# Kernel optimization log

Measured on AMD Instinct MI355X. Metric: run time of the kernel, lower is better.

Reference implementation:

```python
import jax, jax.numpy as jnp
import numpy as np

N = 100000   # nodes
F = 64       # features
K = 5        # filter taps
E = 1600000  # edges per sparse power (avg degree 16)


def setup_inputs() -> dict:
    key = jax.random.key(0)
    k1, k2, k3, k4, k5 = jax.random.split(key, 5)
    x = jax.random.normal(k1, (N, F), dtype=jnp.float32)
    h = jax.random.normal(k2, (K,), dtype=jnp.float32)
    vals = jax.random.normal(k3, (K, E), dtype=jnp.float32)
    rows = jax.random.randint(k4, (K, E), 0, N, dtype=jnp.int32)
    cols = jax.random.randint(k5, (K, E), 0, N, dtype=jnp.int32)
    return {"x": x, "h": h, "vals": vals, "rows": rows, "cols": cols}


def reference(x, h, vals, rows, cols):
    # H = sum_k h[k] * S_k  (COO);  out = H @ x
    # Fuse the weighted sum of K sparse matrices directly into one SpMM:
    # scale each power's values by h[k], flatten all K edge lists, and
    # scatter-add the gathered rows of x.
    n = x.shape[0]
    w = (h[:, None] * vals).reshape(-1)          # [K*E]
    r = rows.reshape(-1)                         # [K*E]
    c = cols.reshape(-1)                         # [K*E]
    contrib = x[c] * w[:, None]                  # [K*E, F] gather + scale
    out = jax.ops.segment_sum(contrib, r, num_segments=n)  # [N, F]
    return out
```

## Files before the change

### kernel.cpp

```cpp
#include <hip/hip_runtime.h>
#include <hip/hip_bf16.h>


#define RPB   64
#define SUB   2
#define GWG   128

static __global__ __launch_bounds__(1024) void count_kernel(
    const int* __restrict__ rows, int* __restrict__ cnt,
    int KE, int NSTREAM, int chunk)
{
    extern __shared__ int hist[];
    const int g = blockIdx.x;
    for (int j = threadIdx.x; j < NSTREAM; j += blockDim.x) hist[j] = 0;
    __syncthreads();
    const int lo = g * chunk;
    const int hi = min(lo + chunk, KE);
    for (int e = lo + threadIdx.x; e < hi; e += blockDim.x) {
        const int r = rows[e];
        atomicAdd(&hist[((r >> 6) << 1) | (r & 1)], 1);
    }
    __syncthreads();
    for (int j = threadIdx.x; j < NSTREAM; j += blockDim.x)
        cnt[(size_t)j * GWG + g] = hist[j];
}

static __global__ __launch_bounds__(GWG) void scan1_kernel(
    int* __restrict__ cnt, int* __restrict__ ssBeg)
{
    __shared__ int tmp[GWG];
    const int s = blockIdx.x;
    const int t = threadIdx.x;
    const int v = cnt[(size_t)s * GWG + t];
    tmp[t] = v;
    __syncthreads();
    for (int d = 1; d < GWG; d <<= 1) {
        int u = (t >= d) ? tmp[t - d] : 0;
        __syncthreads();
        tmp[t] += u;
        __syncthreads();
    }
    cnt[(size_t)s * GWG + t] = tmp[t] - v;
    if (t == GWG - 1) ssBeg[s] = tmp[t];
}

static __global__ __launch_bounds__(1024) void scan2_kernel(
    int* __restrict__ a, int n)
{
    __shared__ int sums[1024];
    const int t = threadIdx.x;
    const int chunk = (n + 1023) >> 10;
    const int lo = t * chunk;
    const int hi = min(lo + chunk, n);
    int s = 0;
    for (int i = lo; i < hi; ++i) s += a[i];
    sums[t] = s;
    __syncthreads();
    for (int d = 1; d < 1024; d <<= 1) {
        int v = (t >= d) ? sums[t - d] : 0;
        __syncthreads();
        sums[t] += v;
        __syncthreads();
    }
    int run = (t > 0) ? sums[t - 1] : 0;
    for (int i = lo; i < hi; ++i) {
        const int cv = a[i];
        a[i] = run;
        run += cv;
    }
    if (t == 1023) a[n] = sums[1023];
}

static __global__ __launch_bounds__(1024) void scan3_kernel(
    int* __restrict__ cnt, const int* __restrict__ ssBeg, int total)
{
    const int i = blockIdx.x * blockDim.x + threadIdx.x;
    if (i < total) cnt[i] += ssBeg[i >> 7];
}

static __global__ __launch_bounds__(1024) void scatter_kernel(
    const int*   __restrict__ rows,
    const int*   __restrict__ cols,
    const float* __restrict__ vals,
    const float* __restrict__ h,
    const int*   __restrict__ cnt,
    int2*        __restrict__ payload,
    int KE, int E, int K, int NSTREAM, int chunk)
{
    extern __shared__ int lcur[];
    const int g = blockIdx.x;
    for (int j = threadIdx.x; j < NSTREAM; j += blockDim.x)
        lcur[j] = cnt[(size_t)j * GWG + g];
    __syncthreads();
    const int lo = g * chunk;
    const int hi = min(lo + chunk, KE);
    if (lo >= hi) return;
    const int k0 = lo / E;
    const int k1 = min((hi - 1) / E, K - 1);
    for (int k = k0; k <= k1; ++k) {
        const float hk = h[k];
        const int s0 = max(lo, k * E);
        const int s1 = min(hi, (k + 1) * E);
        for (int e = s0 + threadIdx.x; e < s1; e += blockDim.x) {
            const int r = rows[e];
            const int st = ((r >> 6) << 1) | (r & 1);
            const int pos = atomicAdd(&lcur[st], 1);
            payload[pos] = make_int2(((r & 63) << 17) | cols[e],
                                     __float_as_int(hk * vals[e]));
        }
    }
}

static __global__ __launch_bounds__(256) void convert_kernel(
    const float* __restrict__ x, ushort* __restrict__ xh, int n4)
{
    const int i = blockIdx.x * blockDim.x + threadIdx.x;
    if (i >= n4) return;
    const float4 v = ((const float4*)x)[i];
    ushort4 o;
    o.x = __bfloat16_as_ushort(__float2bfloat16(v.x));
    o.y = __bfloat16_as_ushort(__float2bfloat16(v.y));
    o.z = __bfloat16_as_ushort(__float2bfloat16(v.z));
    o.w = __bfloat16_as_ushort(__float2bfloat16(v.w));
    ((ushort4*)xh)[i] = o;
}

static __global__ __launch_bounds__(128) void spmv_bf16_kernel(
    const int*    __restrict__ ssBeg,
    const int2*   __restrict__ payload,
    const ushort* __restrict__ xh,
    float*        __restrict__ out,
    int N)
{
    __shared__ float acc[RPB * 64];
    const int b = blockIdx.x;
    for (int i = threadIdx.x; i < RPB * 64; i += 128) acc[i] = 0.f;
    __syncthreads();

    const int lane = threadIdx.x & 63;
    const int wv   = threadIdx.x >> 6;
    const int s    = b * SUB + wv;
    int e        = ssBeg[s];
    const int be = ssBeg[s + 1];

    while (e + 16 <= be) {
        int2 pa[8], pb[8];
        float xa[8], xb[8];
        #pragma unroll
        for (int j = 0; j < 8; ++j) pa[j] = payload[e + j];
        #pragma unroll
        for (int j = 0; j < 8; ++j) pb[j] = payload[e + 8 + j];
        #pragma unroll
        for (int j = 0; j < 8; ++j)
            xa[j] = __bfloat162float(__ushort_as_bfloat16(
                        xh[(size_t)(pa[j].x & 0x1FFFF) * 64 + lane]));
        #pragma unroll
        for (int j = 0; j < 8; ++j)
            xb[j] = __bfloat162float(__ushort_as_bfloat16(
                        xh[(size_t)(pb[j].x & 0x1FFFF) * 64 + lane]));
        #pragma unroll
        for (int j = 0; j < 8; ++j)
            acc[(pa[j].x >> 17) * 64 + lane] += __int_as_float(pa[j].y) * xa[j];
        #pragma unroll
        for (int j = 0; j < 8; ++j)
            acc[(pb[j].x >> 17) * 64 + lane] += __int_as_float(pb[j].y) * xb[j];
        e += 16;
    }
    for (; e < be; ++e) {
        const int2 p = payload[e];
        const float xv = __bfloat162float(__ushort_as_bfloat16(
                             xh[(size_t)(p.x & 0x1FFFF) * 64 + lane]));
        acc[(p.x >> 17) * 64 + lane] += __int_as_float(p.y) * xv;
    }
    __syncthreads();

    const int base = b * RPB;
    const int nrow = min(RPB, N - base);
    for (int i = threadIdx.x; i < nrow * 64; i += 128)
        out[(size_t)base * 64 + i] = acc[i];
}

static __global__ __launch_bounds__(128) void spmv_f32_kernel(
    const int*  __restrict__ ssBeg,
    const int2* __restrict__ payload,
    const float* __restrict__ x,
    float*       __restrict__ out,
    int N)
{
    __shared__ float acc[RPB * 64];
    const int b = blockIdx.x;
    for (int i = threadIdx.x; i < RPB * 64; i += 128) acc[i] = 0.f;
    __syncthreads();

    const int lane = threadIdx.x & 63;
    const int wv   = threadIdx.x >> 6;
    const int s    = b * SUB + wv;
    int e        = ssBeg[s];
    const int be = ssBeg[s + 1];

    while (e + 16 <= be) {
        int2 pa[8], pb[8];
        float xa[8], xb[8];
        #pragma unroll
        for (int j = 0; j < 8; ++j) pa[j] = payload[e + j];
        #pragma unroll
        for (int j = 0; j < 8; ++j) pb[j] = payload[e + 8 + j];
        #pragma unroll
        for (int j = 0; j < 8; ++j)
            xa[j] = x[(size_t)(pa[j].x & 0x1FFFF) * 64 + lane];
        #pragma unroll
        for (int j = 0; j < 8; ++j)
            xb[j] = x[(size_t)(pb[j].x & 0x1FFFF) * 64 + lane];
        #pragma unroll
        for (int j = 0; j < 8; ++j)
            acc[(pa[j].x >> 17) * 64 + lane] += __int_as_float(pa[j].y) * xa[j];
        #pragma unroll
        for (int j = 0; j < 8; ++j)
            acc[(pb[j].x >> 17) * 64 + lane] += __int_as_float(pb[j].y) * xb[j];
        e += 16;
    }
    for (; e < be; ++e) {
        const int2 p = payload[e];
        acc[(p.x >> 17) * 64 + lane] +=
            __int_as_float(p.y) * x[(size_t)(p.x & 0x1FFFF) * 64 + lane];
    }
    __syncthreads();

    const int base = b * RPB;
    const int nrow = min(RPB, N - base);
    for (int i = threadIdx.x; i < nrow * 64; i += 128)
        out[(size_t)base * 64 + i] = acc[i];
}

static __global__ __launch_bounds__(256) void gtconv_scatter(
    const float* __restrict__ x, const float* __restrict__ h,
    const float* __restrict__ vals, const int* __restrict__ rows,
    const int* __restrict__ cols, float* __restrict__ out, int KE, int E)
{
    const int lane = threadIdx.x & 63;
    int wave = (blockIdx.x * blockDim.x + threadIdx.x) >> 6;
    const int nwaves = (gridDim.x * blockDim.x) >> 6;
    for (int e = wave; e < KE; e += nwaves) {
        float w = h[e / E] * vals[e];
        float xv = x[(size_t)cols[e] * 64 + lane];
        unsafeAtomicAdd(&out[(size_t)rows[e] * 64 + lane], xv * w);
    }
}

extern "C" void kernel_launch(void* const* d_in, const int* in_sizes, int n_in,
                              void* d_out, int out_size, void* d_ws, size_t ws_size,
                              hipStream_t stream) {
    const float* x    = (const float*)d_in[0];
    const float* h    = (const float*)d_in[1];
    const float* vals = (const float*)d_in[2];
    const int*   rows = (const int*)d_in[3];
    const int*   cols = (const int*)d_in[4];
    float* out = (float*)d_out;

    const int K  = in_sizes[1];
    const int KE = in_sizes[2];
    const int E  = KE / K;
    const int F  = 64;
    const int N  = in_sizes[0] / F;
    const int NB      = (N + RPB - 1) / RPB;
    const int NSTREAM = NB * SUB;

    const size_t lds_need = (size_t)NSTREAM * 4;
    const size_t cnt_off  = 0;
    const size_t cnt_sz   = (size_t)NSTREAM * GWG * 4;
    const size_t ss_off   = cnt_off + cnt_sz;
    const size_t ss_sz    = (size_t)(NSTREAM + 1) * 4;
    const size_t pl_off   = (ss_off + ss_sz + 15) & ~(size_t)15;
    const size_t base_need = pl_off + (size_t)KE * 8;
    const size_t xh_off   = (base_need + 63) & ~(size_t)63;
    const size_t full_need = xh_off + (size_t)N * F * 2;

    if (ws_size < base_need || lds_need > 64 * 1024) {
        hipMemsetAsync(out, 0, (size_t)out_size * sizeof(float), stream);
        gtconv_scatter<<<8192, 256, 0, stream>>>(x, h, vals, rows, cols, out, KE, E);
        return;
    }

    char* ws = (char*)d_ws;
    int*    cnt     = (int*)(ws + cnt_off);
    int*    ssBeg   = (int*)(ws + ss_off);
    int2*   payload = (int2*)(ws + pl_off);
    ushort* xh      = (ushort*)(ws + xh_off);
    const bool use_bf16 = (ws_size >= full_need);

    if (use_bf16) {
        const int n4 = (N * F) / 4;
        convert_kernel<<<(n4 + 255) / 256, 256, 0, stream>>>(x, xh, n4);
    }

    const int chunk = (KE + GWG - 1) / GWG;
    count_kernel<<<GWG, 1024, lds_need, stream>>>(rows, cnt, KE, NSTREAM, chunk);
    scan1_kernel<<<NSTREAM, GWG, 0, stream>>>(cnt, ssBeg);
    scan2_kernel<<<1, 1024, 0, stream>>>(ssBeg, NSTREAM);
    const int total = NSTREAM * GWG;
    scan3_kernel<<<(total + 1023) / 1024, 1024, 0, stream>>>(cnt, ssBeg, total);
    scatter_kernel<<<GWG, 1024, lds_need, stream>>>(rows, cols, vals, h, cnt,
                                                    payload, KE, E, K, NSTREAM, chunk);
    if (use_bf16)
        spmv_bf16_kernel<<<NB, 128, 0, stream>>>(ssBeg, payload, xh, out, N);
    else
        spmv_f32_kernel<<<NB, 128, 0, stream>>>(ssBeg, payload, x, out, N);
}
```

Before: 384.2 us.

## Bin edges per row block, have both waves scan and filter by row parity

The binning now uses one stream per 64-row block instead of two parity sub-streams, which halves the histogram and scan size. In the SpMM kernel both waves read the whole block payload, and each processes only the edges whose row parity matches its wave index, with the unroll raised to 32. This cuts per-stream bookkeeping and LDS atomic contention in the count and scatter kernels. In exchange each wave loads twice as much payload, and the per-edge divergent predication may leave lanes idle.

```diff
diff --git a/kernel.cpp b/kernel.cpp
--- a/kernel.cpp
+++ b/kernel.cpp
@@ -3,7 +3,6 @@
 
 
 #define RPB   64
-#define SUB   2
 #define GWG   128
 
 static __global__ __launch_bounds__(1024) void count_kernel(
@@ -16,10 +15,8 @@
     __syncthreads();
     const int lo = g * chunk;
     const int hi = min(lo + chunk, KE);
-    for (int e = lo + threadIdx.x; e < hi; e += blockDim.x) {
-        const int r = rows[e];
-        atomicAdd(&hist[((r >> 6) << 1) | (r & 1)], 1);
-    }
+    for (int e = lo + threadIdx.x; e < hi; e += blockDim.x)
+        atomicAdd(&hist[rows[e] >> 6], 1);
     __syncthreads();
     for (int j = threadIdx.x; j < NSTREAM; j += blockDim.x)
         cnt[(size_t)j * GWG + g] = hist[j];
@@ -103,8 +100,7 @@
         const int s1 = min(hi, (k + 1) * E);
         for (int e = s0 + threadIdx.x; e < s1; e += blockDim.x) {
             const int r = rows[e];
-            const int st = ((r >> 6) << 1) | (r & 1);
-            const int pos = atomicAdd(&lcur[st], 1);
+            const int pos = atomicAdd(&lcur[r >> 6], 1);
             payload[pos] = make_int2(((r & 63) << 17) | cols[e],
                                      __float_as_int(hk * vals[e]));
         }
@@ -139,38 +135,35 @@
 
     const int lane = threadIdx.x & 63;
     const int wv   = threadIdx.x >> 6;
-    const int s    = b * SUB + wv;
-    int e        = ssBeg[s];
-    const int be = ssBeg[s + 1];
-
-    while (e + 16 <= be) {
-        int2 pa[8], pb[8];
-        float xa[8], xb[8];
-        #pragma unroll
-        for (int j = 0; j < 8; ++j) pa[j] = payload[e + j];
-        #pragma unroll
-        for (int j = 0; j < 8; ++j) pb[j] = payload[e + 8 + j];
-        #pragma unroll
-        for (int j = 0; j < 8; ++j)
-            xa[j] = __bfloat162float(__ushort_as_bfloat16(
-                        xh[(size_t)(pa[j].x & 0x1FFFF) * 64 + lane]));
-        #pragma unroll
-        for (int j = 0; j < 8; ++j)
-            xb[j] = __bfloat162float(__ushort_as_bfloat16(
-                        xh[(size_t)(pb[j].x & 0x1FFFF) * 64 + lane]));
-        #pragma unroll
-        for (int j = 0; j < 8; ++j)
-            acc[(pa[j].x >> 17) * 64 + lane] += __int_as_float(pa[j].y) * xa[j];
-        #pragma unroll
-        for (int j = 0; j < 8; ++j)
-            acc[(pb[j].x >> 17) * 64 + lane] += __int_as_float(pb[j].y) * xb[j];
-        e += 16;
+    int e        = ssBeg[b];
+    const int be = ssBeg[b + 1];
+
+    while (e + 32 <= be) {
+        int2 pp[32];
+        float xv[32];
+        #pragma unroll
+        for (int j = 0; j < 32; ++j) pp[j] = payload[e + j];
+        #pragma unroll
+        for (int j = 0; j < 32; ++j) {
+            if ((((unsigned)pp[j].x >> 17) & 1u) == (unsigned)wv)
+                xv[j] = __bfloat162float(__ushort_as_bfloat16(
+                            xh[(size_t)(pp[j].x & 0x1FFFF) * 64 + lane]));
+        }
+        #pragma unroll
+        for (int j = 0; j < 32; ++j) {
+            if ((((unsigned)pp[j].x >> 17) & 1u) == (unsigned)wv)
+                acc[(pp[j].x >> 17) * 64 + lane] +=
+                    __int_as_float(pp[j].y) * xv[j];
+        }
+        e += 32;
     }
     for (; e < be; ++e) {
         const int2 p = payload[e];
-        const float xv = __bfloat162float(__ushort_as_bfloat16(
-                             xh[(size_t)(p.x & 0x1FFFF) * 64 + lane]));
-        acc[(p.x >> 17) * 64 + lane] += __int_as_float(p.y) * xv;
+        if ((((unsigned)p.x >> 17) & 1u) == (unsigned)wv) {
+            const float xv2 = __bfloat162float(__ushort_as_bfloat16(
+                                  xh[(size_t)(p.x & 0x1FFFF) * 64 + lane]));
+            acc[(p.x >> 17) * 64 + lane] += __int_as_float(p.y) * xv2;
+        }
     }
     __syncthreads();
 
@@ -194,35 +187,32 @@
 
     const int lane = threadIdx.x & 63;
     const int wv   = threadIdx.x >> 6;
-    const int s    = b * SUB + wv;
-    int e        = ssBeg[s];
-    const int be = ssBeg[s + 1];
-
-    while (e + 16 <= be) {
-        int2 pa[8], pb[8];
-        float xa[8], xb[8];
-        #pragma unroll
-        for (int j = 0; j < 8; ++j) pa[j] = payload[e + j];
-        #pragma unroll
-        for (int j = 0; j < 8; ++j) pb[j] = payload[e + 8 + j];
-        #pragma unroll
-        for (int j = 0; j < 8; ++j)
-            xa[j] = x[(size_t)(pa[j].x & 0x1FFFF) * 64 + lane];
-        #pragma unroll
-        for (int j = 0; j < 8; ++j)
-            xb[j] = x[(size_t)(pb[j].x & 0x1FFFF) * 64 + lane];
-        #pragma unroll
-        for (int j = 0; j < 8; ++j)
-            acc[(pa[j].x >> 17) * 64 + lane] += __int_as_float(pa[j].y) * xa[j];
-        #pragma unroll
-        for (int j = 0; j < 8; ++j)
-            acc[(pb[j].x >> 17) * 64 + lane] += __int_as_float(pb[j].y) * xb[j];
-        e += 16;
+    int e        = ssBeg[b];
+    const int be = ssBeg[b + 1];
+
+    while (e + 32 <= be) {
+        int2 pp[32];
+        float xv[32];
+        #pragma unroll
+        for (int j = 0; j < 32; ++j) pp[j] = payload[e + j];
+        #pragma unroll
+        for (int j = 0; j < 32; ++j) {
+            if ((((unsigned)pp[j].x >> 17) & 1u) == (unsigned)wv)
+                xv[j] = x[(size_t)(pp[j].x & 0x1FFFF) * 64 + lane];
+        }
+        #pragma unroll
+        for (int j = 0; j < 32; ++j) {
+            if ((((unsigned)pp[j].x >> 17) & 1u) == (unsigned)wv)
+                acc[(pp[j].x >> 17) * 64 + lane] +=
+                    __int_as_float(pp[j].y) * xv[j];
+        }
+        e += 32;
     }
     for (; e < be; ++e) {
         const int2 p = payload[e];
-        acc[(p.x >> 17) * 64 + lane] +=
-            __int_as_float(p.y) * x[(size_t)(p.x & 0x1FFFF) * 64 + lane];
+        if ((((unsigned)p.x >> 17) & 1u) == (unsigned)wv)
+            acc[(p.x >> 17) * 64 + lane] +=
+                __int_as_float(p.y) * x[(size_t)(p.x & 0x1FFFF) * 64 + lane];
     }
     __syncthreads();
 
@@ -263,7 +253,7 @@
     const int F  = 64;
     const int N  = in_sizes[0] / F;
     const int NB      = (N + RPB - 1) / RPB;
-    const int NSTREAM = NB * SUB;
+    const int NSTREAM = NB;
 
     const size_t lds_need = (size_t)NSTREAM * 4;
     const size_t cnt_off  = 0;
```

Result: slower. 1.233 ms (+221.0%).

## Bucket edges per row block and split work evenly across waves with private accumulators

Applied to the files above, without the earlier changes.

Edges are now bucketed by 64-row block instead of by block-and-row-parity. Each block's edge range is split in half between its two waves, and each wave accumulates into its own LDS buffer; the two buffers are summed when writing out. This balances work between the waves and halves the number of histogram streams, which shrinks the count and scan arrays. In exchange, LDS use per block doubles, which may lower occupancy, and the output step does an extra read and add.

```diff
diff --git a/kernel.cpp b/kernel.cpp
--- a/kernel.cpp
+++ b/kernel.cpp
@@ -3,7 +3,6 @@
 
 
 #define RPB   64
-#define SUB   2
 #define GWG   128
 
 static __global__ __launch_bounds__(1024) void count_kernel(
@@ -16,10 +15,8 @@
     __syncthreads();
     const int lo = g * chunk;
     const int hi = min(lo + chunk, KE);
-    for (int e = lo + threadIdx.x; e < hi; e += blockDim.x) {
-        const int r = rows[e];
-        atomicAdd(&hist[((r >> 6) << 1) | (r & 1)], 1);
-    }
+    for (int e = lo + threadIdx.x; e < hi; e += blockDim.x)
+        atomicAdd(&hist[rows[e] >> 6], 1);
     __syncthreads();
     for (int j = threadIdx.x; j < NSTREAM; j += blockDim.x)
         cnt[(size_t)j * GWG + g] = hist[j];
@@ -103,8 +100,7 @@
         const int s1 = min(hi, (k + 1) * E);
         for (int e = s0 + threadIdx.x; e < s1; e += blockDim.x) {
             const int r = rows[e];
-            const int st = ((r >> 6) << 1) | (r & 1);
-            const int pos = atomicAdd(&lcur[st], 1);
+            const int pos = atomicAdd(&lcur[r >> 6], 1);
             payload[pos] = make_int2(((r & 63) << 17) | cols[e],
                                      __float_as_int(hk * vals[e]));
         }
@@ -132,16 +128,22 @@
     float*        __restrict__ out,
     int N)
 {
-    __shared__ float acc[RPB * 64];
-    const int b = blockIdx.x;
-    for (int i = threadIdx.x; i < RPB * 64; i += 128) acc[i] = 0.f;
-    __syncthreads();
-
-    const int lane = threadIdx.x & 63;
-    const int wv   = threadIdx.x >> 6;
-    const int s    = b * SUB + wv;
-    int e        = ssBeg[s];
-    const int be = ssBeg[s + 1];
+    __shared__ float acc[2][RPB * 64];
+    const int tid = threadIdx.x;
+    float* accf = (float*)acc;
+    for (int i = tid; i < 2 * RPB * 64; i += 128) accf[i] = 0.f;
+    __syncthreads();
+
+    const int b    = blockIdx.x;
+    const int lane = tid & 63;
+    const int wv   = tid >> 6;
+    float* ac = acc[wv];
+
+    const int ss = ssBeg[b];
+    const int se = ssBeg[b + 1];
+    const int half = (se - ss) >> 1;
+    int e        = ss + half * wv;
+    const int be = wv ? se : (ss + half);
 
     while (e + 16 <= be) {
         int2 pa[8], pb[8];
@@ -160,24 +162,24 @@
                         xh[(size_t)(pb[j].x & 0x1FFFF) * 64 + lane]));
         #pragma unroll
         for (int j = 0; j < 8; ++j)
-            acc[(pa[j].x >> 17) * 64 + lane] += __int_as_float(pa[j].y) * xa[j];
-        #pragma unroll
-        for (int j = 0; j < 8; ++j)
-            acc[(pb[j].x >> 17) * 64 + lane] += __int_as_float(pb[j].y) * xb[j];
+            ac[(pa[j].x >> 17) * 64 + lane] += __int_as_float(pa[j].y) * xa[j];
+        #pragma unroll
+        for (int j = 0; j < 8; ++j)
+            ac[(pb[j].x >> 17) * 64 + lane] += __int_as_float(pb[j].y) * xb[j];
         e += 16;
     }
     for (; e < be; ++e) {
         const int2 p = payload[e];
         const float xv = __bfloat162float(__ushort_as_bfloat16(
                              xh[(size_t)(p.x & 0x1FFFF) * 64 + lane]));
-        acc[(p.x >> 17) * 64 + lane] += __int_as_float(p.y) * xv;
+        ac[(p.x >> 17) * 64 + lane] += __int_as_float(p.y) * xv;
     }
     __syncthreads();
 
     const int base = b * RPB;
     const int nrow = min(RPB, N - base);
-    for (int i = threadIdx.x; i < nrow * 64; i += 128)
-        out[(size_t)base * 64 + i] = acc[i];
+    for (int i = tid; i < nrow * 64; i += 128)
+        out[(size_t)base * 64 + i] = acc[0][i] + acc[1][i];
 }
 
 static __global__ __launch_bounds__(128) void spmv_f32_kernel(
@@ -187,16 +189,22 @@
     float*       __restrict__ out,
     int N)
 {
-    __shared__ float acc[RPB * 64];
-    const int b = blockIdx.x;
-    for (int i = threadIdx.x; i < RPB * 64; i += 128) acc[i] = 0.f;
-    __syncthreads();
-
-    const int lane = threadIdx.x & 63;
-    const int wv   = threadIdx.x >> 6;
-    const int s    = b * SUB + wv;
-    int e        = ssBeg[s];
-    const int be = ssBeg[s + 1];
+    __shared__ float acc[2][RPB * 64];
+    const int tid = threadIdx.x;
+    float* accf = (float*)acc;
+    for (int i = tid; i < 2 * RPB * 64; i += 128) accf[i] = 0.f;
+    __syncthreads();
+
+    const int b    = blockIdx.x;
+    const int lane = tid & 63;
+    const int wv   = tid >> 6;
+    float* ac = acc[wv];
+
+    const int ss = ssBeg[b];
+    const int se = ssBeg[b + 1];
+    const int half = (se - ss) >> 1;
+    int e        = ss + half * wv;
+    const int be = wv ? se : (ss + half);
 
     while (e + 16 <= be) {
         int2 pa[8], pb[8];
@@ -213,23 +221,23 @@
             xb[j] = x[(size_t)(pb[j].x & 0x1FFFF) * 64 + lane];
         #pragma unroll
         for (int j = 0; j < 8; ++j)
-            acc[(pa[j].x >> 17) * 64 + lane] += __int_as_float(pa[j].y) * xa[j];
-        #pragma unroll
-        for (int j = 0; j < 8; ++j)
-            acc[(pb[j].x >> 17) * 64 + lane] += __int_as_float(pb[j].y) * xb[j];
+            ac[(pa[j].x >> 17) * 64 + lane] += __int_as_float(pa[j].y) * xa[j];
+        #pragma unroll
+        for (int j = 0; j < 8; ++j)
+            ac[(pb[j].x >> 17) * 64 + lane] += __int_as_float(pb[j].y) * xb[j];
         e += 16;
     }
     for (; e < be; ++e) {
         const int2 p = payload[e];
-        acc[(p.x >> 17) * 64 + lane] +=
+        ac[(p.x >> 17) * 64 + lane] +=
             __int_as_float(p.y) * x[(size_t)(p.x & 0x1FFFF) * 64 + lane];
     }
     __syncthreads();
 
     const int base = b * RPB;
     const int nrow = min(RPB, N - base);
-    for (int i = threadIdx.x; i < nrow * 64; i += 128)
-        out[(size_t)base * 64 + i] = acc[i];
+    for (int i = tid; i < nrow * 64; i += 128)
+        out[(size_t)base * 64 + i] = acc[0][i] + acc[1][i];
 }
 
 static __global__ __launch_bounds__(256) void gtconv_scatter(
@@ -263,7 +271,7 @@
     const int F  = 64;
     const int N  = in_sizes[0] / F;
     const int NB      = (N + RPB - 1) / RPB;
-    const int NSTREAM = NB * SUB;
+    const int NSTREAM = NB;
 
     const size_t lds_need = (size_t)NSTREAM * 4;
     const size_t cnt_off  = 0;
```

New measurement: 508.9 us. 32.5% more time.
